# Performance work log

Measured on AMD Instinct MI355X. Metric: run time of the kernel, lower is better.

Reference implementation:

```python
import jax, jax.numpy as jnp
import numpy as np


def rotate_every_two(x):
    # x: [..., d] with d even; interleave pairs (x1, x2) -> (-x2, x1)
    x1 = x[..., ::2]
    x2 = x[..., 1::2]
    return jnp.stack([-x2, x1], axis=-1).reshape(x.shape)


def theta_shift(x, sin, cos):
    return x * cos + rotate_every_two(x) * sin


def rope_2d(H, W, head_dim, dtype=jnp.float32):
    # angle: [head_dim//4] -> interleaved repeat -> [head_dim//2]
    angle = 1.0 / (10000.0 ** np.linspace(0.0, 1.0, head_dim // 4))
    angle = jnp.asarray(np.repeat(angle, 2), dtype=dtype)  # [d/2]
    ih = jnp.arange(H, dtype=dtype)[:, None] * angle[None, :]  # [H, d/2]
    iw = jnp.arange(W, dtype=dtype)[:, None] * angle[None, :]  # [W, d/2]
    sin_h = jnp.broadcast_to(jnp.sin(ih)[:, None, :], (H, W, head_dim // 2))
    sin_w = jnp.broadcast_to(jnp.sin(iw)[None, :, :], (H, W, head_dim // 2))
    cos_h = jnp.broadcast_to(jnp.cos(ih)[:, None, :], (H, W, head_dim // 2))
    cos_w = jnp.broadcast_to(jnp.cos(iw)[None, :, :], (H, W, head_dim // 2))
    sin = jnp.concatenate([sin_h, sin_w], -1).reshape(H * W, head_dim)
    cos = jnp.concatenate([cos_h, cos_w], -1).reshape(H * W, head_dim)
    return sin, cos


NUM_HEADS = 12


def setup_inputs() -> dict:
    key = jax.random.key(0)
    ks = jax.random.split(key, 11)
    B, N, C = 4, 4096, 768
    s = 1.0 / np.sqrt(C)
    return {
        "query": jax.random.normal(ks[0], (B, N, C), jnp.float32),
        "key": jax.random.normal(ks[1], (B, N, C), jnp.float32),
        "value": jax.random.normal(ks[2], (B, N, C), jnp.float32),
        "Wq": jax.random.normal(ks[3], (C, C), jnp.float32) * s,
        "bq": jax.random.normal(ks[4], (C,), jnp.float32) * s,
        "Wk": jax.random.normal(ks[5], (C, C), jnp.float32) * s,
        "bk": jax.random.normal(ks[6], (C,), jnp.float32) * s,
        "Wv": jax.random.normal(ks[7], (C, C), jnp.float32) * s,
        "bv": jax.random.normal(ks[8], (C,), jnp.float32) * s,
        "Wo": jax.random.normal(ks[9], (C, C), jnp.float32) * s,
        "bo": jax.random.normal(ks[10], (C,), jnp.float32) * s,
        "H": 64,
        "W": 64,
    }


def reference(query, key, value, Wq, bq, Wk, bk, Wv, bv, Wo, bo, H, W):
    B, N, C = query.shape
    h = NUM_HEADS
    d = C // h
    scale = d ** (-0.5)

    def heads(x):  # [B,N,C] -> [B,h,N,d]
        return x.reshape(B, N, h, d).transpose(0, 2, 1, 3)

    q = heads(query @ Wq.T + bq)
    k = heads(key @ Wk.T + bk)
    v = heads(value @ Wv.T + bv)

    q = jax.nn.elu(q) + 1.0
    k = jax.nn.elu(k) + 1.0

    sin, cos = rope_2d(H, W, d, q.dtype)  # each [N, d]

    # z: magnitude term using pre-RoPE feature maps, [B,h,N,1]
    z = jnp.einsum("bhnd,bhd->bhn", q, k.mean(axis=2))[..., None] * scale

    q = theta_shift(q, sin, cos)
    k = theta_shift(k, sin, cos)

    # linear attention: kv = k^T v scaled by scale/N, [B,h,d,d]
    kv = jnp.einsum("bhnd,bhne->bhde", k, v) * (scale / N)
    v_mean = v.mean(axis=2, keepdims=True)  # [B,h,1,d]
    res = jnp.einsum("bhnd,bhde->bhne", q, kv) * (1.0 + 1.0 / (z + 1e-6)) - z * v_mean

    res = res.transpose(0, 2, 1, 3).reshape(B, N, C)
    return res @ Wo.T + bo
```

## Files before the change

kernel.cpp:

```cpp
#include <hip/hip_runtime.h>
#include <math.h>

#define B_SZ   4
#define N_SEQ  4096
#define C_DIM  768
#define NH     12
#define HD     64
#define NBH    (B_SZ*NH)
#define SCALE  0.125f
#define M_ROWS (B_SZ*N_SEQ)

typedef unsigned short u16;
typedef short s16x8 __attribute__((ext_vector_type(8)));
typedef float f32x4 __attribute__((ext_vector_type(4)));
typedef u16 u16x8 __attribute__((ext_vector_type(8)));

__device__ __forceinline__ u16 f2h(float f) { _Float16 h = (_Float16)f; return __builtin_bit_cast(u16, h); }
__device__ __forceinline__ float h2f(u16 u) { return (float)__builtin_bit_cast(_Float16, u); }

__device__ __forceinline__ s16x8 pack_h8(f32x4 x, f32x4 y) {
    s16x8 o;
    #pragma unroll
    for (int i = 0; i < 4; ++i) { o[i] = (short)f2h(x[i]); o[i+4] = (short)f2h(y[i]); }
    return o;
}

typedef const __attribute__((address_space(1))) void GLBV;
typedef __attribute__((address_space(3))) void LDSV;
#define GLDS(g, l) __builtin_amdgcn_global_load_lds((GLBV*)(g), (LDSV*)(l), 16, 0, 0)

__global__ __launch_bounds__(256)
void cvt_w(const float* __restrict__ w0, const float* __restrict__ w1,
           const float* __restrict__ w2, const float* __restrict__ w3,
           u16* __restrict__ o0, u16* __restrict__ o1, u16* __restrict__ o2, u16* __restrict__ o3) {
    size_t i = ((size_t)blockIdx.x * 256 + threadIdx.x) * 8;
    const float* srcs[4] = {w0 + i, w1 + i, w2 + i, w3 + i};
    u16* dsts[4] = {o0 + i, o1 + i, o2 + i, o3 + i};
    #pragma unroll
    for (int s = 0; s < 4; ++s) {
        float4 x = *(const float4*)srcs[s];
        float4 y = *(const float4*)(srcs[s] + 4);
        u16x8 o;
        o[0] = f2h(x.x); o[1] = f2h(x.y); o[2] = f2h(x.z); o[3] = f2h(x.w);
        o[4] = f2h(y.x); o[5] = f2h(y.y); o[6] = f2h(y.z); o[7] = f2h(y.w);
        *(u16x8*)dsts[s] = o;
    }
}

__global__ void rope_table_k(const int* __restrict__ dH, const int* __restrict__ dW,
                             float* __restrict__ sin_t, float* __restrict__ cos_t) {
    int idx = blockIdx.x * 256 + threadIdx.x;
    if (idx >= N_SEQ * HD) return;
    int n = idx >> 6, j = idx & 63;
    int Wd = dW[0];
    int hh = n / Wd, ww = n % Wd;
    int jj = j & 31;
    float pos = (j < 32) ? (float)hh : (float)ww;
    float freq = powf(10000.0f, -((float)(jj >> 1) / 15.0f));
    float th = pos * freq;
    sin_t[idx] = sinf(th);
    cos_t[idx] = cosf(th);
}


template<int ACT>
__global__ __launch_bounds__(512)
void gemm_f32a(const float* __restrict__ A, const u16* __restrict__ Bw,
               const float* __restrict__ bias, u16* __restrict__ Cc) {
    constexpr int K = C_DIM, Nn = C_DIM;
    __shared__ __align__(16) float As[128 * 64];
    __shared__ __align__(16) u16  Bs[128 * 64];
    const int t = threadIdx.x;
    const int lane = t & 63, w = t >> 6;
    const int wr = w >> 1, wc = w & 1;
    const int bid = blockIdx.x;
    const int wg = (bid & 7) * 96 + (bid >> 3);
    const int bx = wg % 6, by = wg / 6;
    const int m0 = by * 128, n0 = bx * 128;

    const int ra = lane & 15, kgu = lane >> 4;

    const int arow = w * 4 + kgu;
    const int acolb = ((lane & 15) * 16) ^ ((((w & 1) * 4 + kgu) & 7) << 5);
    const char* gA = (const char*)(A + (size_t)(m0 + arow) * K) + acolb;
    const int brow = w * 8 + (lane >> 3);
    const int bcol = ((lane & 7) * 8) ^ ((lane >> 3) << 3);
    const u16* gB = Bw + (size_t)(n0 + brow) * K + bcol;

    f32x4 acc[2][4] = {};

    for (int k0 = 0; k0 < K; k0 += 64) {
        __syncthreads();
        GLDS(gA,                          &As[(0 * 32 + w * 4) * 64]);
        GLDS(gA + (size_t)32 * K * 4,     &As[(1 * 32 + w * 4) * 64]);
        GLDS(gA + (size_t)64 * K * 4,     &As[(2 * 32 + w * 4) * 64]);
        GLDS(gA + (size_t)96 * K * 4,     &As[(3 * 32 + w * 4) * 64]);
        GLDS(gB,                          &Bs[(0 * 64 + w * 8) * 64]);
        GLDS(gB + (size_t)64 * K,         &Bs[(1 * 64 + w * 8) * 64]);
        gA += 256; gB += 64;
        __syncthreads();
        #pragma unroll
        for (int kk = 0; kk < 2; ++kk) {
            const int fo = (kk * 32 + kgu * 8) ^ ((ra & 7) << 3);
            s16x8 av[2], bv[4];
            #pragma unroll
            for (int i = 0; i < 2; ++i) {
                const float* ap = &As[(wr * 32 + i * 16 + ra) * 64 + fo];
                av[i] = pack_h8(*(const f32x4*)ap, *(const f32x4*)(ap + 4));
            }
            #pragma unroll
            for (int j = 0; j < 4; ++j)
                bv[j] = *(const s16x8*)&Bs[(wc * 64 + j * 16 + ra) * 64 + fo];
            #pragma unroll
            for (int i = 0; i < 2; ++i)
                #pragma unroll
                for (int j = 0; j < 4; ++j)
                    asm("v_mfma_f32_16x16x32_f16 %0, %1, %2, %0"
                        : "+v"(acc[i][j]) : "v"(av[i]), "v"(bv[j]));
        }
    }

    const int cr4 = kgu * 4, cc = ra;
    #pragma unroll
    for (int j = 0; j < 4; ++j) {
        const int col = n0 + wc * 64 + j * 16 + cc;
        const float bj = bias[col];
        #pragma unroll
        for (int i = 0; i < 2; ++i) {
            const int row = m0 + wr * 32 + i * 16 + cr4;
            #pragma unroll
            for (int r = 0; r < 4; ++r) {
                float v = acc[i][j][r] + bj;
                if (ACT) v = (v > 0.f) ? (v + 1.f) : __expf(v);
                Cc[(size_t)(row + r) * Nn + col] = f2h(v);
            }
        }
    }
}

__global__ __launch_bounds__(512)
void gemm_q(const float* __restrict__ A, const u16* __restrict__ Bw,
            const float* __restrict__ bias, const float* __restrict__ km,
            const float* __restrict__ sin_t, const float* __restrict__ cos_t,
            u16* __restrict__ Qr, float* __restrict__ zbuf) {
    constexpr int K = C_DIM, Nn = C_DIM;
    __shared__ __align__(16) float As[128 * 64];
    __shared__ __align__(16) u16  Bs[128 * 64];
    const int t = threadIdx.x;
    const int lane = t & 63, w = t >> 6;
    const int wr = w >> 1, wc = w & 1;
    const int bid = blockIdx.x;
    const int wg = (bid & 7) * 96 + (bid >> 3);
    const int bx = wg % 6, by = wg / 6;
    const int m0 = by * 128, n0 = bx * 128;

    const int ra = lane & 15, kgu = lane >> 4;

    const int arow = w * 4 + kgu;
    const int acolb = ((lane & 15) * 16) ^ ((((w & 1) * 4 + kgu) & 7) << 5);
    const char* gA = (const char*)(A + (size_t)(m0 + arow) * K) + acolb;
    const int brow = w * 8 + (lane >> 3);
    const int bcol = ((lane & 7) * 8) ^ ((lane >> 3) << 3);
    const u16* gB = Bw + (size_t)(n0 + brow) * K + bcol;

    f32x4 acc[2][4] = {};

    for (int k0 = 0; k0 < K; k0 += 64) {
        __syncthreads();
        GLDS(gA,                          &As[(0 * 32 + w * 4) * 64]);
        GLDS(gA + (size_t)32 * K * 4,     &As[(1 * 32 + w * 4) * 64]);
        GLDS(gA + (size_t)64 * K * 4,     &As[(2 * 32 + w * 4) * 64]);
        GLDS(gA + (size_t)96 * K * 4,     &As[(3 * 32 + w * 4) * 64]);
        GLDS(gB,                          &Bs[(0 * 64 + w * 8) * 64]);
        GLDS(gB + (size_t)64 * K,         &Bs[(1 * 64 + w * 8) * 64]);
        gA += 256; gB += 64;
        __syncthreads();
        #pragma unroll
        for (int kk = 0; kk < 2; ++kk) {
            const int fo = (kk * 32 + kgu * 8) ^ ((ra & 7) << 3);
            s16x8 av[2], bv[4];
            #pragma unroll
            for (int i = 0; i < 2; ++i) {
                const float* ap = &As[(wr * 32 + i * 16 + ra) * 64 + fo];
                av[i] = pack_h8(*(const f32x4*)ap, *(const f32x4*)(ap + 4));
            }
            #pragma unroll
            for (int j = 0; j < 4; ++j)
                bv[j] = *(const s16x8*)&Bs[(wc * 64 + j * 16 + ra) * 64 + fo];
            #pragma unroll
            for (int i = 0; i < 2; ++i)
                #pragma unroll
                for (int j = 0; j < 4; ++j)
                    asm("v_mfma_f32_16x16x32_f16 %0, %1, %2, %0"
                        : "+v"(acc[i][j]) : "v"(av[i]), "v"(bv[j]));
        }
    }

    const int cr4 = kgu * 4, cc = ra;
    const int b = m0 >> 12;
    const int h = (n0 >> 6) + wc;
    float kmv[4];
    #pragma unroll
    for (int j = 0; j < 4; ++j) kmv[j] = km[(b * NH + h) * HD + j * 16 + cc];

    #pragma unroll
    for (int i = 0; i < 2; ++i) {
        #pragma unroll
        for (int r = 0; r < 4; ++r) {
            const int row = m0 + wr * 32 + i * 16 + cr4 + r;
            const int n = row & (N_SEQ - 1);
            float q[4], zp = 0.f;
            #pragma unroll
            for (int j = 0; j < 4; ++j) {
                float v = acc[i][j][r] + bias[n0 + wc * 64 + j * 16 + cc];
                v = (v > 0.f) ? (v + 1.f) : __expf(v);
                q[j] = v;
                zp += v * kmv[j];
            }
            zp += __shfl_xor(zp, 1); zp += __shfl_xor(zp, 2);
            zp += __shfl_xor(zp, 4); zp += __shfl_xor(zp, 8);
            if (cc == 0) zbuf[((size_t)(b * NH + h)) * N_SEQ + n] = zp * SCALE;
            #pragma unroll
            for (int j = 0; j < 4; ++j) {
                const int d = j * 16 + cc;
                const float p = __shfl_xor(q[j], 1);
                const float rot = (d & 1) ? p : -p;
                const size_t toff = (size_t)n * HD + d;
                const float qr = q[j] * cos_t[toff] + rot * sin_t[toff];
                Qr[(size_t)row * Nn + n0 + wc * 64 + d] = f2h(qr);
            }
        }
    }
}

__global__ __launch_bounds__(512)
void gemm_f16a(const u16* __restrict__ A, const u16* __restrict__ Bw,
               const float* __restrict__ bias, float* __restrict__ Cc) {
    constexpr int K = C_DIM, Nn = C_DIM;
    __shared__ __align__(16) u16 As[128 * 64];
    __shared__ __align__(16) u16 Bs[128 * 64];
    const int t = threadIdx.x;
    const int lane = t & 63, w = t >> 6;
    const int wr = w >> 1, wc = w & 1;
    const int bid = blockIdx.x;
    const int wg = (bid & 7) * 96 + (bid >> 3);
    const int bx = wg % 6, by = wg / 6;
    const int m0 = by * 128, n0 = bx * 128;

    const int ra = lane & 15, kgu = lane >> 4;

    const int row0 = w * 8 + (lane >> 3);
    const int col0 = ((lane & 7) * 8) ^ ((lane >> 3) << 3);
    const u16* gA = A + (size_t)(m0 + row0) * K + col0;
    const u16* gB = Bw + (size_t)(n0 + row0) * K + col0;

    f32x4 acc[2][4] = {};

    for (int k0 = 0; k0 < K; k0 += 64) {
        __syncthreads();
        GLDS(gA,                      &As[(0 * 64 + w * 8) * 64]);
        GLDS(gA + (size_t)64 * K,     &As[(1 * 64 + w * 8) * 64]);
        GLDS(gB,                      &Bs[(0 * 64 + w * 8) * 64]);
        GLDS(gB + (size_t)64 * K,     &Bs[(1 * 64 + w * 8) * 64]);
        gA += 64; gB += 64;
        __syncthreads();
        #pragma unroll
        for (int kk = 0; kk < 2; ++kk) {
            const int fo = (kk * 32 + kgu * 8) ^ ((ra & 7) << 3);
            s16x8 av[2], bv[4];
            #pragma unroll
            for (int i = 0; i < 2; ++i)
                av[i] = *(const s16x8*)&As[(wr * 32 + i * 16 + ra) * 64 + fo];
            #pragma unroll
            for (int j = 0; j < 4; ++j)
                bv[j] = *(const s16x8*)&Bs[(wc * 64 + j * 16 + ra) * 64 + fo];
            #pragma unroll
            for (int i = 0; i < 2; ++i)
                #pragma unroll
                for (int j = 0; j < 4; ++j)
                    asm("v_mfma_f32_16x16x32_f16 %0, %1, %2, %0"
                        : "+v"(acc[i][j]) : "v"(av[i]), "v"(bv[j]));
        }
    }

    const int cr4 = kgu * 4, cc = ra;
    #pragma unroll
    for (int j = 0; j < 4; ++j) {
        const int col = n0 + wc * 64 + j * 16 + cc;
        const float bj = bias[col];
        #pragma unroll
        for (int i = 0; i < 2; ++i) {
            const int row = m0 + wr * 32 + i * 16 + cr4;
            #pragma unroll
            for (int r = 0; r < 4; ++r)
                Cc[(size_t)(row + r) * Nn + col] = acc[i][j][r] + bj;
        }
    }
}

__global__ __launch_bounds__(256)
void kv_partial(const u16* __restrict__ Kb, const u16* __restrict__ Vb,
                const float* __restrict__ sin_t, const float* __restrict__ cos_t,
                float* __restrict__ pkv, float* __restrict__ pk, float* __restrict__ pv) {
    int bh = blockIdx.x, chunk = blockIdx.y;
    int b = bh / NH, h = bh % NH;
    int t = threadIdx.x, tx = t & 15, ty = t >> 4;
    __shared__ float Kt[32][64];
    __shared__ float Vt[32][64];
    float acc[4][4] = {};
    float sk[8] = {}, sv[8] = {};
    int n0 = chunk * 128;
    int lr = t >> 3, lc = (t & 7) * 8;
    for (int nc = 0; nc < 128; nc += 32) {
        int n = n0 + nc + lr;
        size_t off = ((size_t)b * N_SEQ + n) * C_DIM + h * HD + lc;
        size_t toff = (size_t)n * HD + lc;
        u16x8 k8 = *(const u16x8*)&Kb[off];
        u16x8 v8 = *(const u16x8*)&Vb[off];
        float kf[8], vf[8];
        #pragma unroll
        for (int i = 0; i < 8; ++i) {
            kf[i] = h2f(k8[i]); vf[i] = h2f(v8[i]);
            sk[i] += kf[i]; sv[i] += vf[i];
        }
        float4 s1 = *(const float4*)&sin_t[toff];
        float4 s2 = *(const float4*)&sin_t[toff + 4];
        float4 c1 = *(const float4*)&cos_t[toff];
        float4 c2 = *(const float4*)&cos_t[toff + 4];
        float sn[8] = {s1.x, s1.y, s1.z, s1.w, s2.x, s2.y, s2.z, s2.w};
        float cs[8] = {c1.x, c1.y, c1.z, c1.w, c2.x, c2.y, c2.z, c2.w};
        float kr[8];
        #pragma unroll
        for (int e = 0; e < 8; e += 2) {
            kr[e]   = kf[e] * cs[e]     - kf[e+1] * sn[e];
            kr[e+1] = kf[e+1] * cs[e+1] + kf[e]   * sn[e+1];
        }
        __syncthreads();
        #pragma unroll
        for (int i = 0; i < 8; ++i) { Kt[lr][lc + i] = kr[i]; Vt[lr][lc + i] = vf[i]; }
        __syncthreads();
        #pragma unroll
        for (int nn = 0; nn < 32; ++nn) {
            float a[4], bb[4];
            #pragma unroll
            for (int i = 0; i < 4; ++i) a[i] = Kt[nn][ty * 4 + i];
            #pragma unroll
            for (int j = 0; j < 4; ++j) bb[j] = Vt[nn][tx * 4 + j];
            #pragma unroll
            for (int i = 0; i < 4; ++i)
                #pragma unroll
                for (int j = 0; j < 4; ++j)
                    acc[i][j] += a[i] * bb[j];
        }
    }
    size_t obase = ((size_t)bh * 32 + chunk) * 4096;
    #pragma unroll
    for (int i = 0; i < 4; ++i)
        #pragma unroll
        for (int j = 0; j < 4; ++j)
            pkv[obase + (ty * 4 + i) * 64 + (tx * 4 + j)] = acc[i][j];
    __syncthreads();
    #pragma unroll
    for (int i = 0; i < 8; ++i) { Kt[lr][lc + i] = sk[i]; Vt[lr][lc + i] = sv[i]; }
    __syncthreads();
    if (t < 64) {
        float s1 = 0.f, s2 = 0.f;
        #pragma unroll
        for (int r = 0; r < 32; ++r) { s1 += Kt[r][t]; s2 += Vt[r][t]; }
        pk[((size_t)bh * 32 + chunk) * 64 + t] = s1;
        pv[((size_t)bh * 32 + chunk) * 64 + t] = s2;
    }
}

__global__ __launch_bounds__(256)
void kvred(const float* __restrict__ pkv, const float* __restrict__ pk, const float* __restrict__ pv,
           u16* __restrict__ kvT, float* __restrict__ km, float* __restrict__ vm) {
    int bh = blockIdx.x, t = threadIdx.x;
    int u = blockIdx.y * 256 + t;
    float s = 0.f;
    for (int c = 0; c < 32; ++c) s += pkv[((size_t)bh * 32 + c) * 4096 + u];
    s *= (SCALE / N_SEQ);
    int d = u >> 6, e = u & 63;
    u16 hi = f2h(s);
    u16 lo = f2h(s - h2f(hi));
    kvT[(size_t)bh * 8192 + e * 64 + d] = hi;
    kvT[(size_t)bh * 8192 + 4096 + e * 64 + d] = lo;
    if (blockIdx.y == 0 && t < 128) {
        int which = t >> 6, lane = t & 63;
        const float* src = which ? pv : pk;
        float s2 = 0.f;
        for (int c = 0; c < 32; ++c) s2 += src[((size_t)bh * 32 + c) * 64 + lane];
        (which ? vm : km)[bh * 64 + lane] = s2 * (1.0f / N_SEQ);
    }
}

#define LDQ 72
__global__ __launch_bounds__(256)
void res_mfma(u16* __restrict__ Qr,
              const u16* __restrict__ kvT,
              const float* __restrict__ vmean, const float* __restrict__ zbuf) {
    __shared__ __align__(16) u16 qs[128 * LDQ];
    __shared__ __align__(16) u16 kvs[2][64 * LDQ];
    __shared__ float zs[128];
    __shared__ float vms[64];
    const int bh = blockIdx.x;
    const int b = bh / NH, h = bh % NH;
    const int n0 = blockIdx.y * 128;
    const int t = threadIdx.x;
    const int lane = t & 63, w = t >> 6;

    {
        const int r = t >> 2, c = (t & 3) * 16;
        #pragma unroll
        for (int p = 0; p < 2; ++p) {
            size_t g = (size_t)bh * 8192 + p * 4096 + r * 64 + c;
            *(u16x8*)&kvs[p][r * LDQ + c]     = *(const u16x8*)&kvT[g];
            *(u16x8*)&kvs[p][r * LDQ + c + 8] = *(const u16x8*)&kvT[g + 8];
        }
    }
    if (t < 64) vms[t] = vmean[bh * 64 + t];
    else if (t < 192) zs[t - 64] = zbuf[(size_t)bh * N_SEQ + n0 + (t - 64)];
    #pragma unroll
    for (int ri = 0; ri < 4; ++ri) {
        const int row = ri * 32 + (t >> 3);
        const int c = (t & 7) * 8;
        size_t off = ((size_t)b * N_SEQ + n0 + row) * C_DIM + (size_t)h * HD + c;
        *(u16x8*)&qs[row * LDQ + c] = *(const u16x8*)&Qr[off];
    }
    __syncthreads();

    f32x4 acc[2][4] = {};
    const int ra = lane & 15, kg = (lane >> 4) * 8;
    #pragma unroll
    for (int p = 0; p < 2; ++p) {
        #pragma unroll
        for (int hh = 0; hh < 2; ++hh) {
            s16x8 bv4[4];
            #pragma unroll
            for (int j = 0; j < 4; ++j)
                bv4[j] = *(const s16x8*)&kvs[p][(j * 16 + ra) * LDQ + hh * 32 + kg];
            #pragma unroll
            for (int i = 0; i < 2; ++i) {
                s16x8 av = *(const s16x8*)&qs[(w * 32 + i * 16 + ra) * LDQ + hh * 32 + kg];
                #pragma unroll
                for (int j = 0; j < 4; ++j)
                    asm("v_mfma_f32_16x16x32_f16 %0, %1, %2, %0"
                        : "+v"(acc[i][j]) : "v"(av), "v"(bv4[j]));
            }
        }
    }

    const int cr4 = (lane >> 4) * 4, cc = lane & 15;
    #pragma unroll
    for (int i = 0; i < 2; ++i) {
        #pragma unroll
        for (int j = 0; j < 4; ++j) {
            const int col = j * 16 + cc;
            const float vmc = vms[col];
            #pragma unroll
            for (int r = 0; r < 4; ++r) {
                const int row = w * 32 + i * 16 + cr4 + r;
                const float z = zs[row];
                const float v = acc[i][j][r] * (1.0f + 1.0f / (z + 1e-6f)) - z * vmc;
                Qr[((size_t)b * N_SEQ + n0 + row) * C_DIM + (size_t)h * HD + col] = f2h(v);
            }
        }
    }
}

extern "C" void kernel_launch(void* const* d_in, const int* in_sizes, int n_in,
                              void* d_out, int out_size, void* d_ws, size_t ws_size,
                              hipStream_t stream) {
    const float* query = (const float*)d_in[0];
    const float* key   = (const float*)d_in[1];
    const float* value = (const float*)d_in[2];
    const float* Wq = (const float*)d_in[3];
    const float* bq = (const float*)d_in[4];
    const float* Wk = (const float*)d_in[5];
    const float* bk = (const float*)d_in[6];
    const float* Wv = (const float*)d_in[7];
    const float* bv = (const float*)d_in[8];
    const float* Wo = (const float*)d_in[9];
    const float* bo = (const float*)d_in[10];
    const int* dH = (const int*)d_in[11];
    const int* dW = (const int*)d_in[12];
    float* out = (float*)d_out;

    const size_t mc = (size_t)M_ROWS * C_DIM;
    const size_t wsz = (size_t)C_DIM * C_DIM;

    u16* ws16 = (u16*)d_ws;
    u16* Qr  = ws16;
    u16* Kb  = Qr + mc;
    u16* Vb  = Kb + mc;
    u16* wqb = Vb + mc;
    u16* wkb = wqb + wsz;
    u16* wvb = wkb + wsz;
    u16* wob = wvb + wsz;
    u16* kvT = wob + wsz;

    float* wsf = (float*)(kvT + (size_t)NBH * 8192);
    float* sin_t = wsf;
    float* cos_t = sin_t + (size_t)N_SEQ * HD;
    float* pk    = cos_t + (size_t)N_SEQ * HD;
    float* pv    = pk + (size_t)NBH * 32 * 64;
    float* km    = pv + (size_t)NBH * 32 * 64;
    float* vm    = km + NBH * 64;
    float* zbuf  = vm + NBH * 64;
    float* pkv   = zbuf + (size_t)NBH * N_SEQ;

    cvt_w<<<dim3(288), dim3(256), 0, stream>>>(Wq, Wk, Wv, Wo, wqb, wkb, wvb, wob);
    rope_table_k<<<dim3(1024), dim3(256), 0, stream>>>(dH, dW, sin_t, cos_t);

    gemm_f32a<1><<<dim3(768), dim3(512), 0, stream>>>(key,   wkb, bk, Kb);
    gemm_f32a<0><<<dim3(768), dim3(512), 0, stream>>>(value, wvb, bv, Vb);

    kv_partial<<<dim3(NBH, 32), dim3(256), 0, stream>>>(Kb, Vb, sin_t, cos_t, pkv, pk, pv);
    kvred<<<dim3(NBH, 16), dim3(256), 0, stream>>>(pkv, pk, pv, kvT, km, vm);

    gemm_q<<<dim3(768), dim3(512), 0, stream>>>(query, wqb, bq, km, sin_t, cos_t, Qr, zbuf);

    res_mfma<<<dim3(NBH, N_SEQ / 128), dim3(256), 0, stream>>>(Qr, kvT, vm, zbuf);

    gemm_f16a<<<dim3(768), dim3(512), 0, stream>>>(Qr, wob, bo, out);
}
```

Before: 216.5 us.

## Prefetch A tiles into registers and convert to fp16 before LDS store

All three GEMM kernels stop loading the A operand with direct global-to-LDS loads. Each thread now prefetches its slice of the next A tile into registers while MFMAs run on the current tile, then writes it to shared memory. In the fp32-input GEMMs the fp16 conversion happens once at store time rather than on every LDS read, which halves A's shared-memory footprint and read traffic. The cost is extra registers for the prefetch buffers, and the A load is no longer asynchronous, so its latency has to be hidden by the compute phase.

```diff
diff --git a/kernel.cpp b/kernel.cpp
--- a/kernel.cpp
+++ b/kernel.cpp
@@ -68,8 +68,8 @@
 void gemm_f32a(const float* __restrict__ A, const u16* __restrict__ Bw,
                const float* __restrict__ bias, u16* __restrict__ Cc) {
     constexpr int K = C_DIM, Nn = C_DIM;
-    __shared__ __align__(16) float As[128 * 64];
-    __shared__ __align__(16) u16  Bs[128 * 64];
+    __shared__ __align__(16) u16 As[128 * 64];
+    __shared__ __align__(16) u16 Bs[128 * 64];
     const int t = threadIdx.x;
     const int lane = t & 63, w = t >> 6;
     const int wr = w >> 1, wc = w & 1;
@@ -80,34 +80,43 @@
 
     const int ra = lane & 15, kgu = lane >> 4;
 
-    const int arow = w * 4 + kgu;
-    const int acolb = ((lane & 15) * 16) ^ ((((w & 1) * 4 + kgu) & 7) << 5);
-    const char* gA = (const char*)(A + (size_t)(m0 + arow) * K) + acolb;
+    const int srow = t >> 2, sqtr = t & 3;
+    const float* gAr = A + (size_t)(m0 + srow) * K + sqtr * 16;
+    u16* wA0 = &As[srow * 64 + (((sqtr * 2 + 0) ^ (srow & 7)) << 3)];
+    u16* wA1 = &As[srow * 64 + (((sqtr * 2 + 1) ^ (srow & 7)) << 3)];
+
     const int brow = w * 8 + (lane >> 3);
     const int bcol = ((lane & 7) * 8) ^ ((lane >> 3) << 3);
     const u16* gB = Bw + (size_t)(n0 + brow) * K + bcol;
 
     f32x4 acc[2][4] = {};
+    f32x4 pa0, pa1, pa2, pa3;
+    pa0 = *(const f32x4*)(gAr + 0);
+    pa1 = *(const f32x4*)(gAr + 4);
+    pa2 = *(const f32x4*)(gAr + 8);
+    pa3 = *(const f32x4*)(gAr + 12);
 
     for (int k0 = 0; k0 < K; k0 += 64) {
         __syncthreads();
-        GLDS(gA,                          &As[(0 * 32 + w * 4) * 64]);
-        GLDS(gA + (size_t)32 * K * 4,     &As[(1 * 32 + w * 4) * 64]);
-        GLDS(gA + (size_t)64 * K * 4,     &As[(2 * 32 + w * 4) * 64]);
-        GLDS(gA + (size_t)96 * K * 4,     &As[(3 * 32 + w * 4) * 64]);
-        GLDS(gB,                          &Bs[(0 * 64 + w * 8) * 64]);
-        GLDS(gB + (size_t)64 * K,         &Bs[(1 * 64 + w * 8) * 64]);
-        gA += 256; gB += 64;
-        __syncthreads();
+        *(s16x8*)wA0 = pack_h8(pa0, pa1);
+        *(s16x8*)wA1 = pack_h8(pa2, pa3);
+        GLDS(gB,                  &Bs[(0 * 64 + w * 8) * 64]);
+        GLDS(gB + (size_t)64 * K, &Bs[(1 * 64 + w * 8) * 64]);
+        gB += 64;
+        __syncthreads();
+        if (k0 + 64 < K) {
+            pa0 = *(const f32x4*)(gAr + k0 + 64);
+            pa1 = *(const f32x4*)(gAr + k0 + 68);
+            pa2 = *(const f32x4*)(gAr + k0 + 72);
+            pa3 = *(const f32x4*)(gAr + k0 + 76);
+        }
         #pragma unroll
         for (int kk = 0; kk < 2; ++kk) {
             const int fo = (kk * 32 + kgu * 8) ^ ((ra & 7) << 3);
             s16x8 av[2], bv[4];
             #pragma unroll
-            for (int i = 0; i < 2; ++i) {
-                const float* ap = &As[(wr * 32 + i * 16 + ra) * 64 + fo];
-                av[i] = pack_h8(*(const f32x4*)ap, *(const f32x4*)(ap + 4));
-            }
+            for (int i = 0; i < 2; ++i)
+                av[i] = *(const s16x8*)&As[(wr * 32 + i * 16 + ra) * 64 + fo];
             #pragma unroll
             for (int j = 0; j < 4; ++j)
                 bv[j] = *(const s16x8*)&Bs[(wc * 64 + j * 16 + ra) * 64 + fo];
@@ -144,8 +153,8 @@
             const float* __restrict__ sin_t, const float* __restrict__ cos_t,
             u16* __restrict__ Qr, float* __restrict__ zbuf) {
     constexpr int K = C_DIM, Nn = C_DIM;
-    __shared__ __align__(16) float As[128 * 64];
-    __shared__ __align__(16) u16  Bs[128 * 64];
+    __shared__ __align__(16) u16 As[128 * 64];
+    __shared__ __align__(16) u16 Bs[128 * 64];
     const int t = threadIdx.x;
     const int lane = t & 63, w = t >> 6;
     const int wr = w >> 1, wc = w & 1;
@@ -156,34 +165,43 @@
 
     const int ra = lane & 15, kgu = lane >> 4;
 
-    const int arow = w * 4 + kgu;
-    const int acolb = ((lane & 15) * 16) ^ ((((w & 1) * 4 + kgu) & 7) << 5);
-    const char* gA = (const char*)(A + (size_t)(m0 + arow) * K) + acolb;
+    const int srow = t >> 2, sqtr = t & 3;
+    const float* gAr = A + (size_t)(m0 + srow) * K + sqtr * 16;
+    u16* wA0 = &As[srow * 64 + (((sqtr * 2 + 0) ^ (srow & 7)) << 3)];
+    u16* wA1 = &As[srow * 64 + (((sqtr * 2 + 1) ^ (srow & 7)) << 3)];
+
     const int brow = w * 8 + (lane >> 3);
     const int bcol = ((lane & 7) * 8) ^ ((lane >> 3) << 3);
     const u16* gB = Bw + (size_t)(n0 + brow) * K + bcol;
 
     f32x4 acc[2][4] = {};
+    f32x4 pa0, pa1, pa2, pa3;
+    pa0 = *(const f32x4*)(gAr + 0);
+    pa1 = *(const f32x4*)(gAr + 4);
+    pa2 = *(const f32x4*)(gAr + 8);
+    pa3 = *(const f32x4*)(gAr + 12);
 
     for (int k0 = 0; k0 < K; k0 += 64) {
         __syncthreads();
-        GLDS(gA,                          &As[(0 * 32 + w * 4) * 64]);
-        GLDS(gA + (size_t)32 * K * 4,     &As[(1 * 32 + w * 4) * 64]);
-        GLDS(gA + (size_t)64 * K * 4,     &As[(2 * 32 + w * 4) * 64]);
-        GLDS(gA + (size_t)96 * K * 4,     &As[(3 * 32 + w * 4) * 64]);
-        GLDS(gB,                          &Bs[(0 * 64 + w * 8) * 64]);
-        GLDS(gB + (size_t)64 * K,         &Bs[(1 * 64 + w * 8) * 64]);
-        gA += 256; gB += 64;
-        __syncthreads();
+        *(s16x8*)wA0 = pack_h8(pa0, pa1);
+        *(s16x8*)wA1 = pack_h8(pa2, pa3);
+        GLDS(gB,                  &Bs[(0 * 64 + w * 8) * 64]);
+        GLDS(gB + (size_t)64 * K, &Bs[(1 * 64 + w * 8) * 64]);
+        gB += 64;
+        __syncthreads();
+        if (k0 + 64 < K) {
+            pa0 = *(const f32x4*)(gAr + k0 + 64);
+            pa1 = *(const f32x4*)(gAr + k0 + 68);
+            pa2 = *(const f32x4*)(gAr + k0 + 72);
+            pa3 = *(const f32x4*)(gAr + k0 + 76);
+        }
         #pragma unroll
         for (int kk = 0; kk < 2; ++kk) {
             const int fo = (kk * 32 + kgu * 8) ^ ((ra & 7) << 3);
             s16x8 av[2], bv[4];
             #pragma unroll
-            for (int i = 0; i < 2; ++i) {
-                const float* ap = &As[(wr * 32 + i * 16 + ra) * 64 + fo];
-                av[i] = pack_h8(*(const f32x4*)ap, *(const f32x4*)(ap + 4));
-            }
+            for (int i = 0; i < 2; ++i)
+                av[i] = *(const s16x8*)&As[(wr * 32 + i * 16 + ra) * 64 + fo];
             #pragma unroll
             for (int j = 0; j < 4; ++j)
                 bv[j] = *(const s16x8*)&Bs[(wc * 64 + j * 16 + ra) * 64 + fo];
@@ -249,21 +267,31 @@
 
     const int ra = lane & 15, kgu = lane >> 4;
 
-    const int row0 = w * 8 + (lane >> 3);
-    const int col0 = ((lane & 7) * 8) ^ ((lane >> 3) << 3);
-    const u16* gA = A + (size_t)(m0 + row0) * K + col0;
-    const u16* gB = Bw + (size_t)(n0 + row0) * K + col0;
+    const int srow = t >> 2, sqtr = t & 3;
+    const u16* gAr = A + (size_t)(m0 + srow) * K + sqtr * 16;
+    u16* wA0 = &As[srow * 64 + (((sqtr * 2 + 0) ^ (srow & 7)) << 3)];
+    u16* wA1 = &As[srow * 64 + (((sqtr * 2 + 1) ^ (srow & 7)) << 3)];
+
+    const int brow = w * 8 + (lane >> 3);
+    const int bcol = ((lane & 7) * 8) ^ ((lane >> 3) << 3);
+    const u16* gB = Bw + (size_t)(n0 + brow) * K + bcol;
 
     f32x4 acc[2][4] = {};
+    u16x8 qa0 = *(const u16x8*)(gAr + 0);
+    u16x8 qa1 = *(const u16x8*)(gAr + 8);
 
     for (int k0 = 0; k0 < K; k0 += 64) {
         __syncthreads();
-        GLDS(gA,                      &As[(0 * 64 + w * 8) * 64]);
-        GLDS(gA + (size_t)64 * K,     &As[(1 * 64 + w * 8) * 64]);
-        GLDS(gB,                      &Bs[(0 * 64 + w * 8) * 64]);
-        GLDS(gB + (size_t)64 * K,     &Bs[(1 * 64 + w * 8) * 64]);
-        gA += 64; gB += 64;
-        __syncthreads();
+        *(u16x8*)wA0 = qa0;
+        *(u16x8*)wA1 = qa1;
+        GLDS(gB,                  &Bs[(0 * 64 + w * 8) * 64]);
+        GLDS(gB + (size_t)64 * K, &Bs[(1 * 64 + w * 8) * 64]);
+        gB += 64;
+        __syncthreads();
+        if (k0 + 64 < K) {
+            qa0 = *(const u16x8*)(gAr + k0 + 64);
+            qa1 = *(const u16x8*)(gAr + k0 + 72);
+        }
         #pragma unroll
         for (int kk = 0; kk < 2; ++kk) {
             const int fo = (kk * 32 + kgu * 8) ^ ((ra & 7) << 3);
```

Result: slower. 221.4 us (+2.3%).
